# Optimization experiments

Measured on AMD Instinct MI355X. Metric: run time of the kernel, lower is better.

## Reference

```python
import jax, jax.numpy as jnp
import numpy as np

B, T, F = 128, 512, 16   # batch, seq len, n_features
K, PAD, H = 5, 2, 32     # conv kernel, padding, per-feature GRU hidden
NEG = 0.01               # LeakyReLU default negative slope


def setup_inputs() -> dict:
    key = jax.random.key(0)
    ks = iter(jax.random.split(key, 64))

    def u(shape, fan):
        s = 1.0 / np.sqrt(fan)
        return jax.random.uniform(next(ks), shape, jnp.float32, -s, s)

    inp = {}
    inp['x'] = jax.random.normal(next(ks), (B, 2, T), jnp.float32)
    # gru_enc: input=2, hidden=F, unidirectional (torch layout: W_ih [3H,I], W_hh [3H,H])
    inp['enc_Wih'] = u((3 * F, 2), F)
    inp['enc_Whh'] = u((3 * F, F), F)
    inp['enc_bih'] = u((3 * F,), F)
    inp['enc_bhh'] = u((3 * F,), F)
    # last_layers_gru (per feature): input=1, hidden=H, bidirectional
    for d in ('f', 'b'):
        inp[f'g1_Wih_{d}'] = u((F, 3 * H, 1), H)
        inp[f'g1_Whh_{d}'] = u((F, 3 * H, H), H)
        inp[f'g1_bih_{d}'] = u((F, 3 * H), H)
        inp[f'g1_bhh_{d}'] = u((F, 3 * H), H)
    # layers_gru (per feature): input=2H, hidden=H, unidirectional
    inp['g2_Wih'] = u((F, 3 * H, 2 * H), H)
    inp['g2_Whh'] = u((F, 3 * H, H), H)
    inp['g2_bih'] = u((F, 3 * H), H)
    inp['g2_bhh'] = u((F, 3 * H), H)
    # ConvTranspose1d weights, torch layout [C_in, C_out, K]
    inp['w3'] = u((F, 32, 64, K), 32 * K)
    inp['b3'] = u((F, 64), 32 * K)
    inp['w2'] = u((F, 64, 128, K), 64 * K)
    inp['b2'] = u((F, 128), 64 * K)
    inp['w1'] = u((F, 128, 1, K), 128 * K)
    inp['b1'] = u((F, 1), 128 * K)
    return inp


def gru(x, Wih, Whh, bih, bhh):
    # x: [B, T, I] -> [B, T, H]; torch GRU cell math
    Hh = Whh.shape[1]
    xp = jnp.einsum('bti,gi->btg', x, Wih) + bih  # [B,T,3H], input proj for all t

    def step(h, xt):
        g = h @ Whh.T + bhh
        xr, xz, xn = jnp.split(xt, 3, -1)
        hr, hz, hn = jnp.split(g, 3, -1)
        r = jax.nn.sigmoid(xr + hr)
        z = jax.nn.sigmoid(xz + hz)
        n = jnp.tanh(xn + r * hn)
        h = (1 - z) * n + z * h
        return h, h

    h0 = jnp.zeros((x.shape[0], Hh), x.dtype)
    _, ys = jax.lax.scan(step, h0, jnp.swapaxes(xp, 0, 1))
    return jnp.swapaxes(ys, 0, 1)


def bigru(x, Wf, Hf, bif, bhf, Wb, Hb, bib, bhb):
    fwd = gru(x, Wf, Hf, bif, bhf)
    bwd = gru(x[:, ::-1], Wb, Hb, bib, bhb)[:, ::-1]
    return jnp.concatenate([fwd, bwd], -1)


def convT(x, w, b):
    # ConvTranspose1d(stride=1, padding=PAD): x [B,Cin,T], w [Cin,Cout,K]
    wc = jnp.flip(w, -1).transpose(1, 0, 2)  # -> [Cout,Cin,K] cross-correlation kernel
    y = jax.lax.conv_general_dilated(
        x, wc, (1,), [(K - 1 - PAD, K - 1 - PAD)],
        dimension_numbers=('NCH', 'OIH', 'NCH'))
    return y + b[None, :, None]


def reference(x, enc_Wih, enc_Whh, enc_bih, enc_bhh,
              g1_Wih_f, g1_Whh_f, g1_bih_f, g1_bhh_f,
              g1_Wih_b, g1_Whh_b, g1_bih_b, g1_bhh_b,
              g2_Wih, g2_Whh, g2_bih, g2_bhh,
              w3, b3, w2, b2, w1, b1):
    leaky = lambda v: jnp.where(v >= 0, v, NEG * v)
    # encoder GRU over time: x [B,2,T] -> [B,T,F]
    h = gru(jnp.swapaxes(x, 1, 2), enc_Wih, enc_Whh, enc_bih, enc_bhh)

    def per_feature(xi, W1f, H1f, bi1f, bh1f, W1b, H1b, bi1b, bh1b,
                    W2, H2, bi2, bh2, w3_, b3_, w2_, b2_, w1_, b1_):
        # xi: [B,T] single feature channel
        u = bigru(xi[..., None], W1f, H1f, bi1f, bh1f, W1b, H1b, bi1b, bh1b)  # [B,T,2H]
        u = gru(u, W2, H2, bi2, bh2)        # [B,T,H]
        u = jnp.swapaxes(u, 1, 2)           # [B,H,T]
        u = leaky(convT(u, w3_, b3_))       # [B,64,T]
        u = leaky(convT(u, w2_, b2_))       # [B,128,T]
        u = leaky(convT(u, w1_, b1_))       # [B,1,T]
        return u[:, 0]                      # [B,T]

    feats = jnp.moveaxis(h, 2, 0)           # [F,B,T]
    out = jax.vmap(per_feature)(feats,
                                g1_Wih_f, g1_Whh_f, g1_bih_f, g1_bhh_f,
                                g1_Wih_b, g1_Whh_b, g1_bih_b, g1_bhh_b,
                                g2_Wih, g2_Whh, g2_bih, g2_bhh,
                                w3, b3, w2, b2, w1, b1)  # [F,B,T]
    return jnp.moveaxis(out, 0, 2)          # [B,T,F]
```

## Files before the change

### kernel.cpp

```cpp
#include <hip/hip_runtime.h>
#include <math.h>

#define BB 128
#define TT 512
#define FF 16

typedef _Float16 half8 __attribute__((ext_vector_type(8)));
typedef float floatx4 __attribute__((ext_vector_type(4)));

union HU { uint4 u; half8 h; };

__device__ __forceinline__ float bf2f(unsigned short u){
  union { unsigned int i; float f; } c; c.i = ((unsigned int)u) << 16; return c.f;
}
__device__ __forceinline__ unsigned short f2bf(float f){
  union { float f; unsigned int i; } c; c.f = f;
  unsigned int x = c.i;
  unsigned int r = (x + 0x7fffu + ((x >> 16) & 1u)) >> 16;
  return (unsigned short)r;
}
__device__ __forceinline__ float sigm(float x){
  return __builtin_amdgcn_rcpf(1.f + __expf(-x));
}
__device__ __forceinline__ float tanh_fast(float x){
  x = fminf(15.f, fmaxf(-15.f, x));
  float e = __expf(-2.f*x);
  return (1.f - e)*__builtin_amdgcn_rcpf(1.f + e);
}
__device__ __forceinline__ float lrelu(float v){ return v >= 0.f ? v : 0.01f*v; }

__device__ __forceinline__ unsigned int packhl(float v){
  _Float16 hh = (_Float16)v;
  float hf = (float)hh;
  _Float16 hl = (_Float16)(v - hf);
  union { _Float16 h; unsigned short s; } a, b;
  a.h = hh; b.h = hl;
  return (unsigned int)a.s | ((unsigned int)b.s << 16);
}

__device__ __forceinline__ void unpackAB(uint4 P0, uint4 P1, HU& Ah, HU& Al){
  Ah.u.x = (P0.x & 0xffffu) | (P0.y << 16);
  Ah.u.y = (P0.z & 0xffffu) | (P0.w << 16);
  Ah.u.z = (P1.x & 0xffffu) | (P1.y << 16);
  Ah.u.w = (P1.z & 0xffffu) | (P1.w << 16);
  Al.u.x = (P0.x >> 16) | (P0.y & 0xffff0000u);
  Al.u.y = (P0.z >> 16) | (P0.w & 0xffff0000u);
  Al.u.z = (P1.x >> 16) | (P1.y & 0xffff0000u);
  Al.u.w = (P1.z >> 16) | (P1.w & 0xffff0000u);
}

#define MFMA16(A,B,C) __builtin_amdgcn_mfma_f32_16x16x32_f16((A),(B),(C),0,0,0)

__global__ __launch_bounds__(256) void fill_kernel(unsigned short* out, int n, float v){
  int i = blockIdx.x*256 + threadIdx.x;
  if (i < n) out[i] = f2bf(v);
}

__global__ __launch_bounds__(256) void detect1_kernel(const unsigned short* x, float* maxbuf){
  __shared__ float red[256];
  const int base = blockIdx.x*4096 + threadIdx.x*16;
  const uint4* p = (const uint4*)(x + base);
  uint4 a = p[0], b = p[1];
  unsigned int ws[8] = {a.x,a.y,a.z,a.w,b.x,b.y,b.z,b.w};
  float m = 0.f;
  #pragma unroll
  for (int i=0;i<8;i++){
    float v0 = fabsf(bf2f((unsigned short)(ws[i] & 0xffffu)));
    float v1 = fabsf(bf2f((unsigned short)(ws[i] >> 16)));
    if (!isfinite(v0)) v0 = 3e38f;
    if (!isfinite(v1)) v1 = 3e38f;
    m = fmaxf(m, fmaxf(v0, v1));
  }
  red[threadIdx.x] = m; __syncthreads();
  for (int s=128; s>0; s>>=1){
    if (threadIdx.x < s) red[threadIdx.x] = fmaxf(red[threadIdx.x], red[threadIdx.x+s]);
    __syncthreads();
  }
  if (threadIdx.x == 0) maxbuf[blockIdx.x] = red[0];
}
__global__ __launch_bounds__(64) void detect2_kernel(const float* maxbuf, int* flag){
  if (threadIdx.x == 0){
    float m = 0.f;
    for (int i=0;i<32;i++) m = fmaxf(m, maxbuf[i]);
    *flag = (m < 1e4f) ? 1 : 0;
  }
}

struct CvtArgs { const void* p[23]; int sz[23]; int ofs[23]; };

__global__ __launch_bounds__(256) void convert_kernel(CvtArgs a, const int* flag, float* dst){
  const int i = blockIdx.x;
  const int n = a.sz[i];
  const int start = blockIdx.y * 16384;
  if (start >= n) return;
  const int end = (start + 16384 < n) ? start + 16384 : n;
  float* d = dst + a.ofs[i];
  const int s4 = start >> 2, e4 = end >> 2;
  if (*flag){
    const unsigned short* s = (const unsigned short*)a.p[i];
    for (int e = s4 + threadIdx.x; e < e4; e += 256){
      uint2 w = *(const uint2*)(s + 4*e);
      float4 o;
      o.x = bf2f((unsigned short)(w.x & 0xffffu));
      o.y = bf2f((unsigned short)(w.x >> 16));
      o.z = bf2f((unsigned short)(w.y & 0xffffu));
      o.w = bf2f((unsigned short)(w.y >> 16));
      *(float4*)(d + 4*e) = o;
    }
  } else {
    const float* s = (const float*)a.p[i];
    for (int e = s4 + threadIdx.x; e < e4; e += 256)
      *(float4*)(d + 4*e) = *(const float4*)(s + 4*e);
  }
}

__global__ __launch_bounds__(256) void prep16_kernel(
    const float* __restrict__ cvt, _Float16* __restrict__ h16,
    int o6, int o10, int o14, int o13, int o17, int o19, int o2)
{
  const int i = blockIdx.x*256 + threadIdx.x;
  const int y = blockIdx.y;
  if (y == 0){ if (i < 49152) h16[i]          = (_Float16)cvt[o6  + i]; }
  else if (y == 1){ if (i < 49152) h16[49152 + i]  = (_Float16)cvt[o10 + i]; }
  else if (y == 2){ if (i < 49152) h16[98304 + i]  = (_Float16)cvt[o14 + i]; }
  else if (y == 3){ if (i < 98304) h16[147456 + i] = (_Float16)cvt[o13 + i]; }
  else if (y == 4){
    if (i < 163840){
      int ci = i & 31, co = (i >> 5) & 63, fj = i >> 11;
      int f = fj / 5, j = fj - 5*f;
      h16[245760 + i] = (_Float16)cvt[o17 + ((f*32 + ci)*64 + co)*5 + j];
    }
  } else if (y == 5){
    if (i < 655360){
      int ci = i & 63, co = (i >> 6) & 127, fj = i >> 13;
      int f = fj / 5, j = fj - 5*f;
      h16[409600 + i] = (_Float16)cvt[o19 + ((f*64 + ci)*128 + co)*5 + j];
    }
  } else {
    if (i < 1536){
      int k = i & 31, row = i >> 5;
      h16[1064960 + i] = (k < 16) ? (_Float16)cvt[o2 + row*16 + k] : (_Float16)0.f;
    }
  }
}

__global__ __launch_bounds__(128) void xt_kernel(const float* __restrict__ cvt, float* __restrict__ xTp){
  const int t = blockIdx.x, b = threadIdx.x;
  xTp[t*BB + b]            = cvt[(b*2 + 0)*TT + t];
  xTp[65536 + t*BB + b]    = cvt[(b*2 + 1)*TT + t];
}

__global__ __launch_bounds__(64) void enc_kernel(
    const float* __restrict__ xTp, const _Float16* __restrict__ whhE,
    const float* __restrict__ Wih, const float* __restrict__ bih,
    const float* __restrict__ bhh, float* __restrict__ xfeatT)
{
  const int b0 = blockIdx.x*16;
  const int l = threadIdx.x, ml = l & 15, q = l >> 4;
  __shared__ __align__(16) _Float16 HpkH[2][16][24];
  __shared__ __align__(16) _Float16 HpkL[2][16][24];
  half8 Bw[3];
  #pragma unroll
  for (int c=0;c<3;c++)
    Bw[c] = *(const half8*)(whhE + (16*c + ml)*32 + 8*q);
  float w0r=Wih[ml*2],      w1r=Wih[ml*2+1],      bir=bih[ml],    bhr=bhh[ml];
  float w0z=Wih[(16+ml)*2], w1z=Wih[(16+ml)*2+1], biz=bih[16+ml], bhz=bhh[16+ml];
  float w0n=Wih[(32+ml)*2], w1n=Wih[(32+ml)*2+1], bin_=bih[32+ml], bhn=bhh[32+ml];
  float hm[4] = {0,0,0,0};
  HU Ah, Al; Ah.u = make_uint4(0,0,0,0); Al.u = Ah.u;
  const floatx4 z4 = {0.f,0.f,0.f,0.f};
  int pp = 0;
  floatx4 x0v = *(const floatx4*)(xTp + b0 + 4*q);
  floatx4 x1v = *(const floatx4*)(xTp + 65536 + b0 + 4*q);
  for (int t=0;t<TT;t++){
    const int tn = (t < 511) ? t+1 : t;
    floatx4 x0n = *(const floatx4*)(xTp + tn*BB + b0 + 4*q);
    floatx4 x1n = *(const floatx4*)(xTp + 65536 + tn*BB + b0 + 4*q);
    floatx4 C[3];
    #pragma unroll
    for (int c=0;c<3;c++){
      C[c] = MFMA16(Al.h, Bw[c], z4);
      C[c] = MFMA16(Ah.h, Bw[c], C[c]);
    }
    float4 hv4;
    #pragma unroll
    for (int r=0;r<4;r++){
      float xb0 = x0v[r], xb1 = x1v[r];
      float rr = sigm(fmaf(w0r,xb0,fmaf(w1r,xb1,bir)) + C[0][r] + bhr);
      float zz = sigm(fmaf(w0z,xb0,fmaf(w1z,xb1,biz)) + C[1][r] + bhz);
      float nn = tanh_fast(fmaf(w0n,xb0,fmaf(w1n,xb1,bin_)) + rr*(C[2][r] + bhn));
      float hn = nn + zz*(hm[r] - nn);
      hm[r] = hn;
      _Float16 hh = (_Float16)hn;
      _Float16 hl = (_Float16)(hn - (float)hh);
      HpkH[pp][4*q + r][ml] = hh;
      HpkL[pp][4*q + r][ml] = hl;
      ((float*)&hv4)[r] = hn;
    }
    *(float4*)(xfeatT + ((size_t)ml*TT + t)*BB + b0 + 4*q) = hv4;
    __syncthreads();
    if (q < 2){
      Ah.u = *(const uint4*)&HpkH[pp][ml][8*q];
      Al.u = *(const uint4*)&HpkL[pp][ml][8*q];
    } else { Ah.u = make_uint4(0,0,0,0); Al.u = Ah.u; }
    pp ^= 1;
    x0v = x0n; x1v = x1n;
  }
}

__global__ __launch_bounds__(128) void g1b_kernel(
    const float* __restrict__ xT, const _Float16* __restrict__ whh_h,
    const float* __restrict__ wih, const float* __restrict__ bih,
    const float* __restrict__ bhh, _Float16* __restrict__ trace)
{
  const int f = blockIdx.x, b0 = blockIdx.y*16;
  const int wid = threadIdx.x >> 6, l = threadIdx.x & 63, ml = l & 15, q = l >> 4;
  __shared__ unsigned int Hpk[2][16][36];
  half8 Bw[3];
  #pragma unroll
  for (int i=0;i<3;i++){
    int tc = 2*i + wid;
    Bw[i] = *(const half8*)(whh_h + (size_t)f*3072 + (16*tc + ml)*32 + 8*q);
  }
  const int j = 16*wid + ml, base = f*96;
  float wir=wih[base+j], wiz=wih[base+32+j], win=wih[base+64+j];
  float br_=bih[base+j]+bhh[base+j];
  float bz_=bih[base+32+j]+bhh[base+32+j];
  float bin_=bih[base+64+j], bhn_=bhh[base+64+j];
  float hm[4] = {0,0,0,0};
  HU Ah, Al; Ah.u = make_uint4(0,0,0,0); Al.u = Ah.u;
  const floatx4 z4 = {0.f,0.f,0.f,0.f};
  int pp = 0;
  floatx4 xv = *(const floatx4*)(xT + ((size_t)f*TT + 511)*BB + b0 + 4*q);
  const int dostore = (wid == (q >> 1));
  for (int s=0;s<512;s++){
    const int t = 511 - s;
    const int tn = (s < 511) ? t-1 : t;
    floatx4 xnx = *(const floatx4*)(xT + ((size_t)f*TT + tn)*BB + b0 + 4*q);
    floatx4 C[3];
    #pragma unroll
    for (int i=0;i<3;i++){
      C[i] = MFMA16(Al.h, Bw[i], z4);
      C[i] = MFMA16(Ah.h, Bw[i], C[i]);
    }
    #pragma unroll
    for (int r=0;r<4;r++){
      float xb = xv[r];
      float rr = sigm(fmaf(wir, xb, br_) + C[0][r]);
      float zz = sigm(fmaf(wiz, xb, bz_) + C[1][r]);
      float nn = tanh_fast(fmaf(win, xb, bin_) + rr*(C[2][r] + bhn_));
      float hn = nn + zz*(hm[r] - nn);
      hm[r] = hn;
      Hpk[pp][4*q + r][j] = packhl(hn);
    }
    __syncthreads();
    {
      uint4 P0 = *(const uint4*)&Hpk[pp][ml][8*q];
      uint4 P1 = *(const uint4*)&Hpk[pp][ml][8*q + 4];
      unpackAB(P0, P1, Ah, Al);
    }
    if (dostore)
      *(uint4*)(trace + (((size_t)(f*BB + b0 + ml))*TT + t)*32 + 8*q) = Ah.u;
    pp ^= 1;
    xv = xnx;
  }
}

__global__ __launch_bounds__(128) void g1bf_kernel(
    const float* __restrict__ xT,
    const _Float16* __restrict__ whhB_h, const float* __restrict__ wihB,
    const float* __restrict__ bihB, const float* __restrict__ bhhB,
    const _Float16* __restrict__ whhF_h, const float* __restrict__ wihF,
    const float* __restrict__ bihF, const float* __restrict__ bhhF,
    _Float16* __restrict__ traceB, _Float16* __restrict__ traceF)
{
  const int f = blockIdx.x, b0 = blockIdx.y*16, dir = blockIdx.z;
  const _Float16* whh_h = dir ? whhF_h : whhB_h;
  const float* wih = dir ? wihF : wihB;
  const float* bih = dir ? bihF : bihB;
  const float* bhh = dir ? bhhF : bhhB;
  _Float16* trace = dir ? traceF : traceB;
  const int wid = threadIdx.x >> 6, l = threadIdx.x & 63, ml = l & 15, q = l >> 4;
  __shared__ __align__(16) _Float16 HpkH[2][16][40];
  __shared__ __align__(16) _Float16 HpkL[2][16][40];
  half8 Bw[3];
  #pragma unroll
  for (int i=0;i<3;i++){
    int tc = 2*i + wid;
    Bw[i] = *(const half8*)(whh_h + (size_t)f*3072 + (16*tc + ml)*32 + 8*q);
  }
  const int j = 16*wid + ml, base = f*96;
  float wir=wih[base+j], wiz=wih[base+32+j], win=wih[base+64+j];
  float br_=bih[base+j]+bhh[base+j];
  float bz_=bih[base+32+j]+bhh[base+32+j];
  float bin_=bih[base+64+j], bhn_=bhh[base+64+j];
  float hm[4] = {0,0,0,0};
  HU Ah, Al; Ah.u = make_uint4(0,0,0,0); Al.u = Ah.u;
  const floatx4 z4 = {0.f,0.f,0.f,0.f};
  int pp = 0;
  const int tfirst = dir ? 0 : 511;
  floatx4 xv = *(const floatx4*)(xT + ((size_t)f*TT + tfirst)*BB + b0 + 4*q);
  const int dostore = (wid == (q >> 1));
  for (int s=0;s<512;s++){
    const int t  = dir ? s : 511 - s;
    const int sn = (s < 511) ? s+1 : s;
    const int tn = dir ? sn : 511 - sn;
    floatx4 xnx = *(const floatx4*)(xT + ((size_t)f*TT + tn)*BB + b0 + 4*q);
    floatx4 C[3];
    #pragma unroll
    for (int i=0;i<3;i++){
      C[i] = MFMA16(Al.h, Bw[i], z4);
      C[i] = MFMA16(Ah.h, Bw[i], C[i]);
    }
    #pragma unroll
    for (int r=0;r<4;r++){
      float xb = xv[r];
      float rr = sigm(fmaf(wir, xb, br_) + C[0][r]);
      float zz = sigm(fmaf(wiz, xb, bz_) + C[1][r]);
      float nn = tanh_fast(fmaf(win, xb, bin_) + rr*(C[2][r] + bhn_));
      float hn = nn + zz*(hm[r] - nn);
      hm[r] = hn;
      _Float16 hh = (_Float16)hn;
      _Float16 hl = (_Float16)(hn - (float)hh);
      HpkH[pp][4*q + r][j] = hh;
      HpkL[pp][4*q + r][j] = hl;
    }
    __syncthreads();
    Ah.u = *(const uint4*)&HpkH[pp][ml][8*q];
    Al.u = *(const uint4*)&HpkL[pp][ml][8*q];
    if (dostore)
      *(uint4*)(trace + (((size_t)(f*BB + b0 + ml))*TT + t)*32 + 8*q) = Ah.u;
    pp ^= 1;
    xv = xnx;
  }
}

__global__ __launch_bounds__(128) void g2_kernel(
    const float* __restrict__ xT,
    const _Float16* __restrict__ wh1_h, const float* __restrict__ wih1,
    const float* __restrict__ bih1, const float* __restrict__ bhh1,
    const _Float16* __restrict__ wh2_h, const _Float16* __restrict__ w2i_h,
    const float* __restrict__ bih2, const float* __restrict__ bhh2,
    _Float16* __restrict__ trace)
{
  const int f = blockIdx.x, b0 = blockIdx.y*16;
  const int wid = threadIdx.x >> 6, l = threadIdx.x & 63, ml = l & 15, q = l >> 4;
  __shared__ unsigned int Hpk1[2][16][36];
  __shared__ unsigned int Hpk2[2][16][36];
  half8 B1[3], Bh2[3], Bx0[3], Bx1[3];
  #pragma unroll
  for (int i=0;i<3;i++){
    int tc = 2*i + wid;
    B1[i]  = *(const half8*)(wh1_h + (size_t)f*3072 + (16*tc + ml)*32 + 8*q);
    Bh2[i] = *(const half8*)(wh2_h + (size_t)f*3072 + (16*tc + ml)*32 + 8*q);
    Bx0[i] = *(const half8*)(w2i_h + (size_t)f*6144 + (16*tc + ml)*64 + 8*q);
    Bx1[i] = *(const half8*)(w2i_h + (size_t)f*6144 + (16*tc + ml)*64 + 32 + 8*q);
  }
  const int j = 16*wid + ml, base = f*96;
  float wir=wih1[base+j], wiz=wih1[base+32+j], win=wih1[base+64+j];
  float br1_=bih1[base+j]+bhh1[base+j];
  float bz1_=bih1[base+32+j]+bhh1[base+32+j];
  float bin1_=bih1[base+64+j], bhn1_=bhh1[base+64+j];
  float br2_=bih2[base+j]+bhh2[base+j];
  float bz2_=bih2[base+32+j]+bhh2[base+32+j];
  float bin2_=bih2[base+64+j], bhn2_=bhh2[base+64+j];
  float h1[4] = {0,0,0,0};
  float h2[4] = {0,0,0,0};
  HU A1h, A1l, A2h, A2l;
  A1h.u = make_uint4(0,0,0,0); A1l.u = A1h.u; A2h.u = A1h.u; A2l.u = A1h.u;
  const floatx4 z4 = {0.f,0.f,0.f,0.f};
  const size_t rowb = ((size_t)(f*BB + b0 + ml))*TT;
  const int dostore = (wid == (q >> 1));

  {
    floatx4 x0v = *(const floatx4*)(xT + (size_t)f*TT*BB + b0 + 4*q);
    #pragma unroll
    for (int r=0;r<4;r++){
      float xb = x0v[r];
      float rr = sigm(fmaf(wir, xb, br1_));
      float zz = sigm(fmaf(wiz, xb, bz1_));
      float nn = tanh_fast(fmaf(win, xb, bin1_) + rr*bhn1_);
      float hn = (1.f - zz)*nn;
      h1[r] = hn;
      Hpk1[0][4*q + r][j] = packhl(hn);
    }
    __syncthreads();
    uint4 P0 = *(const uint4*)&Hpk1[0][ml][8*q];
    uint4 P1 = *(const uint4*)&Hpk1[0][ml][8*q + 4];
    unpackAB(P0, P1, A1h, A1l);
  }
  int pp = 1;
  uint4 Ub = *(const uint4*)(trace + (rowb + 0)*32 + 8*q);
  floatx4 xv = *(const floatx4*)(xT + ((size_t)f*TT + 1)*BB + b0 + 4*q);
  for (int t=0;t<512;t++){
    const int tn1 = (t < 511) ? t+1 : t;
    const int tn2 = (t < 510) ? t+2 : 511;
    uint4 Ubn = *(const uint4*)(trace + (rowb + tn1)*32 + 8*q);
    floatx4 xnx = *(const floatx4*)(xT + ((size_t)f*TT + tn2)*BB + b0 + 4*q);
    floatx4 C1[3];
    #pragma unroll
    for (int i=0;i<3;i++){
      C1[i] = MFMA16(A1l.h, B1[i], z4);
      C1[i] = MFMA16(A1h.h, B1[i], C1[i]);
    }
    HU Abw; Abw.u = Ub;
    floatx4 Cr, Cz, Cnh, Cnx;
    Cr = MFMA16(A2l.h, Bh2[0], z4); Cr = MFMA16(A2h.h, Bh2[0], Cr);
    Cr = MFMA16(A1l.h, Bx0[0], Cr); Cr = MFMA16(A1h.h, Bx0[0], Cr);
    Cr = MFMA16(Abw.h, Bx1[0], Cr);
    Cz = MFMA16(A2l.h, Bh2[1], z4); Cz = MFMA16(A2h.h, Bh2[1], Cz);
    Cz = MFMA16(A1l.h, Bx0[1], Cz); Cz = MFMA16(A1h.h, Bx0[1], Cz);
    Cz = MFMA16(Abw.h, Bx1[1], Cz);
    Cnh = MFMA16(A2l.h, Bh2[2], z4); Cnh = MFMA16(A2h.h, Bh2[2], Cnh);
    Cnx = MFMA16(A1l.h, Bx0[2], z4); Cnx = MFMA16(A1h.h, Bx0[2], Cnx);
    Cnx = MFMA16(Abw.h, Bx1[2], Cnx);
    #pragma unroll
    for (int r=0;r<4;r++){
      float xb = xv[r];
      float rr1 = sigm(fmaf(wir, xb, br1_) + C1[0][r]);
      float zz1 = sigm(fmaf(wiz, xb, bz1_) + C1[1][r]);
      float nn1 = tanh_fast(fmaf(win, xb, bin1_) + rr1*(C1[2][r] + bhn1_));
      float hn1 = nn1 + zz1*(h1[r] - nn1);
      h1[r] = hn1;
      Hpk1[pp][4*q + r][j] = packhl(hn1);

      float rr2 = sigm(Cr[r] + br2_);
      float zz2 = sigm(Cz[r] + bz2_);
      float nn2 = tanh_fast(Cnx[r] + bin2_ + rr2*(Cnh[r] + bhn2_));
      float hn2 = nn2 + zz2*(h2[r] - nn2);
      h2[r] = hn2;
      Hpk2[pp][4*q + r][j] = packhl(hn2);
    }
    __syncthreads();
    {
      uint4 P0 = *(const uint4*)&Hpk1[pp][ml][8*q];
      uint4 P1 = *(const uint4*)&Hpk1[pp][ml][8*q + 4];
      unpackAB(P0, P1, A1h, A1l);
      uint4 Q0 = *(const uint4*)&Hpk2[pp][ml][8*q];
      uint4 Q1 = *(const uint4*)&Hpk2[pp][ml][8*q + 4];
      unpackAB(Q0, Q1, A2h, A2l);
    }
    if (dostore)
      *(uint4*)(trace + (rowb + t)*32 + 8*q) = A2h.u;
    Ub = Ubn; xv = xnx; pp ^= 1;
  }
}

__global__ __launch_bounds__(128) void g2f_kernel(
    const _Float16* __restrict__ wh2_h, const _Float16* __restrict__ w2i_h,
    const float* __restrict__ bih2, const float* __restrict__ bhh2,
    const _Float16* __restrict__ traceF, _Float16* __restrict__ traceB)
{
  const int f = blockIdx.x, b0 = blockIdx.y*16;
  const int wid = threadIdx.x >> 6, l = threadIdx.x & 63, ml = l & 15, q = l >> 4;
  __shared__ __align__(16) _Float16 HpkH[2][16][40];
  __shared__ __align__(16) _Float16 HpkL[2][16][40];
  half8 Bh2[3], Bx0[3], Bx1[3];
  #pragma unroll
  for (int i=0;i<3;i++){
    int tc = 2*i + wid;
    Bh2[i] = *(const half8*)(wh2_h + (size_t)f*3072 + (16*tc + ml)*32 + 8*q);
    Bx0[i] = *(const half8*)(w2i_h + (size_t)f*6144 + (16*tc + ml)*64 + 8*q);
    Bx1[i] = *(const half8*)(w2i_h + (size_t)f*6144 + (16*tc + ml)*64 + 32 + 8*q);
  }
  const int j = 16*wid + ml, base = f*96;
  float br2_=bih2[base+j]+bhh2[base+j];
  float bz2_=bih2[base+32+j]+bhh2[base+32+j];
  float bin2_=bih2[base+64+j], bhn2_=bhh2[base+64+j];
  float h2[4] = {0,0,0,0};
  HU A2h, A2l; A2h.u = make_uint4(0,0,0,0); A2l.u = A2h.u;
  const floatx4 z4 = {0.f,0.f,0.f,0.f};
  const size_t rowb = ((size_t)(f*BB + b0 + ml))*TT;
  const int dostore = (wid == (q >> 1));
  int pp = 0;
  uint4 F0 = *(const uint4*)(traceF + (rowb + 0)*32 + 8*q);
  uint4 F1 = *(const uint4*)(traceF + (rowb + 1)*32 + 8*q);
  uint4 B0 = *(const uint4*)(traceB + (rowb + 0)*32 + 8*q);
  uint4 B1 = *(const uint4*)(traceB + (rowb + 1)*32 + 8*q);
  for (int t=0;t<512;t++){
    const int tn = (t < 510) ? t+2 : 511;
    uint4 F2 = *(const uint4*)(traceF + (rowb + tn)*32 + 8*q);
    uint4 B2 = *(const uint4*)(traceB + (rowb + tn)*32 + 8*q);
    HU AF; AF.u = F0;
    HU AB; AB.u = B0;
    floatx4 Cr, Cz, Cnh, Cnx;
    {
      floatx4 CrA = MFMA16(A2l.h, Bh2[0], z4); CrA = MFMA16(A2h.h, Bh2[0], CrA);
      floatx4 CrB = MFMA16(AF.h, Bx0[0], z4);  CrB = MFMA16(AB.h, Bx1[0], CrB);
      Cr = CrA + CrB;
      floatx4 CzA = MFMA16(A2l.h, Bh2[1], z4); CzA = MFMA16(A2h.h, Bh2[1], CzA);
      floatx4 CzB = MFMA16(AF.h, Bx0[1], z4);  CzB = MFMA16(AB.h, Bx1[1], CzB);
      Cz = CzA + CzB;
      Cnh = MFMA16(A2l.h, Bh2[2], z4); Cnh = MFMA16(A2h.h, Bh2[2], Cnh);
      Cnx = MFMA16(AF.h, Bx0[2], z4);  Cnx = MFMA16(AB.h, Bx1[2], Cnx);
    }
    #pragma unroll
    for (int r=0;r<4;r++){
      float rr2 = sigm(Cr[r] + br2_);
      float zz2 = sigm(Cz[r] + bz2_);
      float nn2 = tanh_fast(Cnx[r] + bin2_ + rr2*(Cnh[r] + bhn2_));
      float hn2 = nn2 + zz2*(h2[r] - nn2);
      h2[r] = hn2;
      _Float16 hh = (_Float16)hn2;
      _Float16 hl = (_Float16)(hn2 - (float)hh);
      HpkH[pp][4*q + r][j] = hh;
      HpkL[pp][4*q + r][j] = hl;
    }
    __syncthreads();
    A2h.u = *(const uint4*)&HpkH[pp][ml][8*q];
    A2l.u = *(const uint4*)&HpkL[pp][ml][8*q];
    if (dostore)
      *(uint4*)(traceB + (rowb + t)*32 + 8*q) = A2h.u;
    F0 = F1; F1 = F2; B0 = B1; B1 = B2; pp ^= 1;
  }
}

#define UTP 40
#define C3P 72
#define C2P 136
__global__ __launch_bounds__(256) void conv_kernel(
    const _Float16* __restrict__ u2,
    const _Float16* __restrict__ w3T, const float* __restrict__ b3,
    const _Float16* __restrict__ w2T, const float* __restrict__ b2,
    const float* __restrict__ w1, const float* __restrict__ b1,
    void* __restrict__ outv, const int* __restrict__ flag)
{
  const int t0 = blockIdx.x * 64;
  const int b  = blockIdx.y;
  const int f  = blockIdx.z;
  const int tid = threadIdx.x;
  const int w = tid >> 6, l = tid & 63, ml = l & 15, q = l >> 4;

  __shared__ __align__(16) _Float16 utb[84][UTP];
  __shared__ __align__(16) _Float16 c3T[84][C3P];
  __shared__ __align__(16) _Float16 c2T[68][C2P];
  __shared__ float red[4][64];

  const _Float16* urow = u2 + ((size_t)(f*BB + b)*TT)*32;
  const floatx4 z4 = {0.f,0.f,0.f,0.f};

  for (int k = tid; k < 76*4; k += 256){
    int n = k >> 2, seg = k & 3;
    int tg = t0 - 6 + n;
    uint4 v = make_uint4(0,0,0,0);
    if (tg >= 0 && tg < TT) v = *(const uint4*)(urow + (size_t)tg*32 + seg*8);
    *(uint4*)&utb[n][seg*8] = v;
  }
  __syncthreads();

  {
    half8 A3[5];
    #pragma unroll
    for (int jj=0;jj<5;jj++)
      A3[jj] = *(const half8*)(w3T + (((size_t)f*5 + jj)*64 + 16*w + ml)*32 + 8*q);
    float bv[4];
    #pragma unroll
    for (int r=0;r<4;r++) bv[r] = b3[f*64 + 16*w + 4*q + r];
    #pragma unroll
    for (int nt=0;nt<5;nt++){
      floatx4 acc = z4;
      #pragma unroll
      for (int jj=0;jj<5;jj++){
        half8 Bb = *(const half8*)&utb[16*nt + ml + 4 - jj][8*q];
        acc = MFMA16(A3[jj], Bb, acc);
      }
      int tm = 16*nt + ml;
      if (tm < 72){
        int G = t0 - 4 + tm;
        unsigned int pk[2];
        #pragma unroll
        for (int h=0;h<2;h++){
          float v0 = acc[2*h]   + bv[2*h];   v0 = lrelu(v0);
          float v1 = acc[2*h+1] + bv[2*h+1]; v1 = lrelu(v1);
          if (G < 0 || G >= TT){ v0 = 0.f; v1 = 0.f; }
          union { _Float16 hh; unsigned short s; } c0, c1;
          c0.hh = (_Float16)v0; c1.hh = (_Float16)v1;
          pk[h] = (unsigned int)c0.s | ((unsigned int)c1.s << 16);
        }
        *(uint2*)&c3T[tm][16*w + 4*q] = make_uint2(pk[0], pk[1]);
      }
    }
  }
  __syncthreads();

  {
    half8 A2f[5][2][2];
    #pragma unroll
    for (int jj=0;jj<5;jj++)
      #pragma unroll
      for (int ch=0;ch<2;ch++)
        #pragma unroll
        for (int mi=0;mi<2;mi++)
          A2f[jj][ch][mi] = *(const half8*)(w2T + (((size_t)f*5 + jj)*128 + 16*(2*w+mi) + ml)*64 + 32*ch + 8*q);
    float bv2[2][4];
    #pragma unroll
    for (int mi=0;mi<2;mi++)
      #pragma unroll
      for (int r=0;r<4;r++) bv2[mi][r] = b2[f*128 + 16*(2*w+mi) + 4*q + r];
    #pragma unroll
    for (int nt=0;nt<5;nt++){
      floatx4 a0 = z4, a1 = z4;
      #pragma unroll
      for (int jj=0;jj<5;jj++){
        #pragma unroll
        for (int ch=0;ch<2;ch++){
          half8 Bb = *(const half8*)&c3T[16*nt + ml + 4 - jj][32*ch + 8*q];
          a0 = MFMA16(A2f[jj][ch][0], Bb, a0);
          a1 = MFMA16(A2f[jj][ch][1], Bb, a1);
        }
      }
      int p = 16*nt + ml;
      if (p < 68){
        int G = t0 - 2 + p;
        #pragma unroll
        for (int mi=0;mi<2;mi++){
          unsigned int pk[2];
          #pragma unroll
          for (int h=0;h<2;h++){
            float v0 = (mi ? a1[2*h]   : a0[2*h])   + bv2[mi][2*h];   v0 = lrelu(v0);
            float v1 = (mi ? a1[2*h+1] : a0[2*h+1]) + bv2[mi][2*h+1]; v1 = lrelu(v1);
            if (G < 0 || G >= TT){ v0 = 0.f; v1 = 0.f; }
            union { _Float16 hh; unsigned short s; } c0, c1;
            c0.hh = (_Float16)v0; c1.hh = (_Float16)v1;
            pk[h] = (unsigned int)c0.s | ((unsigned int)c1.s << 16);
          }
          *(uint2*)&c2T[p][16*(2*w+mi) + 4*q] = make_uint2(pk[0], pk[1]);
        }
      }
    }
  }
  __syncthreads();

  {
    const int tl = tid & 63, cg = tid >> 6;
    const float* wp = w1 + ((size_t)f*128 + cg*32)*5;
    float acc = 0.f;
    #pragma unroll
    for (int jj=0;jj<5;jj++){
      int row = tl + 4 - jj;
      union { uint4 u; _Float16 h[8]; } u0, u1, u2_, u3;
      u0.u  = *(const uint4*)&c2T[row][cg*32];
      u1.u  = *(const uint4*)&c2T[row][cg*32 + 8];
      u2_.u = *(const uint4*)&c2T[row][cg*32 + 16];
      u3.u  = *(const uint4*)&c2T[row][cg*32 + 24];
      #pragma unroll
      for (int i=0;i<8;i++){
        acc = fmaf(wp[i*5 + jj],      (float)u0.h[i],  acc);
        acc = fmaf(wp[(8+i)*5 + jj],  (float)u1.h[i],  acc);
        acc = fmaf(wp[(16+i)*5 + jj], (float)u2_.h[i], acc);
        acc = fmaf(wp[(24+i)*5 + jj], (float)u3.h[i],  acc);
      }
    }
    red[cg][tl] = acc;
  }
  __syncthreads();
  if (tid < 64){
    float s = b1[f] + red[0][tid] + red[1][tid] + red[2][tid] + red[3][tid];
    s = lrelu(s);
    size_t oi = ((size_t)b*TT + t0 + tid)*FF + f;
    if (*flag) ((unsigned short*)outv)[oi] = f2bf(s);
    else       ((float*)outv)[oi] = s;
  }
}

extern "C" void kernel_launch(void* const* d_in, const int* in_sizes, int n_in,
                              void* d_out, int out_size, void* d_ws, size_t ws_size,
                              hipStream_t stream)
{
  static const int esz[23] = {
    131072,
    96, 768, 48, 48,
    1536, 49152, 1536, 1536,
    1536, 49152, 1536, 1536,
    98304, 49152, 1536, 1536,
    163840, 1024,
    655360, 2048,
    10240, 16
  };
  const size_t NEED = (size_t)16*1024*1024 + (size_t)64*1024*1024;

  float diag = 0.f;
  if (n_in != 23) diag = 2000.f + n_in;
  else {
    for (int i=0;i<23;i++) if (in_sizes[i] != esz[i]) { diag = 1000.f + i; break; }
    if (diag == 0.f && ws_size < NEED) diag = 500.f + (float)(ws_size >> 20);
  }
  if (diag != 0.f){
    hipLaunchKernelGGL(fill_kernel, dim3((out_size+255)/256), dim3(256), 0, stream,
                       (unsigned short*)d_out, out_size, diag);
    return;
  }

  float* cvt = (float*)d_ws;
  int* flagp = (int*)((char*)d_ws + (5ull<<20));
  float* maxbuf = (float*)((char*)d_ws + (5ull<<20) + 256);
  _Float16* h16 = (_Float16*)((char*)d_ws + (6ull<<20));
  float* xTp = (float*)((char*)d_ws + (9ull<<20));
  float* xfeatT = (float*)((char*)d_ws + (10ull<<20));
  _Float16* trace = (_Float16*)((char*)d_ws + (14ull<<20));
  _Float16* traceF = (_Float16*)((char*)d_ws + (80ull<<20));
  const bool bigws = (ws_size >= (145ull<<20));

  CvtArgs a;
  int ofs = 0;
  for (int i=0;i<23;i++){ a.p[i] = d_in[i]; a.sz[i] = esz[i]; a.ofs[i] = ofs; ofs += esz[i]; }
  const float* c[23];
  for (int i=0;i<23;i++) c[i] = cvt + a.ofs[i];

  hipLaunchKernelGGL(detect1_kernel, dim3(32), dim3(256), 0, stream,
                     (const unsigned short*)d_in[0], maxbuf);
  hipLaunchKernelGGL(detect2_kernel, dim3(1), dim3(64), 0, stream, maxbuf, flagp);
  hipLaunchKernelGGL(convert_kernel, dim3(23, 40), dim3(256), 0, stream, a, flagp, cvt);
  hipLaunchKernelGGL(prep16_kernel, dim3(2560, 7), dim3(256), 0, stream,
                     cvt, h16, a.ofs[6], a.ofs[10], a.ofs[14], a.ofs[13],
                     a.ofs[17], a.ofs[19], a.ofs[2]);
  hipLaunchKernelGGL(xt_kernel, dim3(TT), dim3(BB), 0, stream, cvt, xTp);
  hipLaunchKernelGGL(enc_kernel, dim3(BB/16), dim3(64), 0, stream,
                     xTp, h16 + 1064960, c[1], c[3], c[4], xfeatT);
  if (bigws){
    hipLaunchKernelGGL(g1bf_kernel, dim3(FF, 8, 2), dim3(128), 0, stream,
                       xfeatT,
                       h16 + 49152, c[9], c[11], c[12],
                       h16 + 0,     c[5], c[7],  c[8],
                       trace, traceF);
    hipLaunchKernelGGL(g2f_kernel, dim3(FF, 8), dim3(128), 0, stream,
                       h16 + 98304, h16 + 147456, c[15], c[16],
                       traceF, trace);
  } else {
    hipLaunchKernelGGL(g1b_kernel, dim3(FF, 8), dim3(128), 0, stream,
                       xfeatT, h16 + 49152, c[9], c[11], c[12], trace);
    hipLaunchKernelGGL(g2_kernel, dim3(FF, 8), dim3(128), 0, stream,
                       xfeatT, h16 + 0, c[5], c[7], c[8],
                       h16 + 98304, h16 + 147456, c[15], c[16], trace);
  }
  hipLaunchKernelGGL(conv_kernel, dim3(TT/64, BB, FF), dim3(256), 0, stream,
                     trace, h16 + 245760, c[18], h16 + 409600, c[20], c[21], c[22],
                     d_out, flagp);
}
```

Measured before the change: 1.325 ms.

## Run recurrent GRU kernels in a single wavefront and drop block barriers

The encoder, g1bf and g2f GRU kernels now run each recurrence in a single 64-lane wavefront. Each lane computes all six gate column tiles itself instead of splitting them across two waves, which removes the per-step __syncthreads and the double-buffered LDS exchange. Every lane also stores the trace, so the dostore predicate is gone. The cost is twice the MFMA and gate math per wave and more registers. Correctness now relies on the single wave staying in lockstep through LDS without explicit wave barriers.

New measurement: 1.579 ms. 1.19x slower.

```diff
diff --git a/kernel.cpp b/kernel.cpp
--- a/kernel.cpp
+++ b/kernel.cpp
@@ -157,8 +157,8 @@
 {
   const int b0 = blockIdx.x*16;
   const int l = threadIdx.x, ml = l & 15, q = l >> 4;
-  __shared__ __align__(16) _Float16 HpkH[2][16][24];
-  __shared__ __align__(16) _Float16 HpkL[2][16][24];
+  __shared__ __align__(16) _Float16 HpkH[16][24];
+  __shared__ __align__(16) _Float16 HpkL[16][24];
   half8 Bw[3];
   #pragma unroll
   for (int c=0;c<3;c++)
@@ -169,7 +169,6 @@
   float hm[4] = {0,0,0,0};
   HU Ah, Al; Ah.u = make_uint4(0,0,0,0); Al.u = Ah.u;
   const floatx4 z4 = {0.f,0.f,0.f,0.f};
-  int pp = 0;
   floatx4 x0v = *(const floatx4*)(xTp + b0 + 4*q);
   floatx4 x1v = *(const floatx4*)(xTp + 65536 + b0 + 4*q);
   for (int t=0;t<TT;t++){
@@ -193,17 +192,15 @@
       hm[r] = hn;
       _Float16 hh = (_Float16)hn;
       _Float16 hl = (_Float16)(hn - (float)hh);
-      HpkH[pp][4*q + r][ml] = hh;
-      HpkL[pp][4*q + r][ml] = hl;
+      HpkH[4*q + r][ml] = hh;
+      HpkL[4*q + r][ml] = hl;
       ((float*)&hv4)[r] = hn;
     }
     *(float4*)(xfeatT + ((size_t)ml*TT + t)*BB + b0 + 4*q) = hv4;
-    __syncthreads();
     if (q < 2){
-      Ah.u = *(const uint4*)&HpkH[pp][ml][8*q];
-      Al.u = *(const uint4*)&HpkL[pp][ml][8*q];
+      Ah.u = *(const uint4*)&HpkH[ml][8*q];
+      Al.u = *(const uint4*)&HpkL[ml][8*q];
     } else { Ah.u = make_uint4(0,0,0,0); Al.u = Ah.u; }
-    pp ^= 1;
     x0v = x0n; x1v = x1n;
   }
 }
@@ -266,7 +263,7 @@
   }
 }
 
-__global__ __launch_bounds__(128) void g1bf_kernel(
+__global__ __launch_bounds__(64) void g1bf_kernel(
     const float* __restrict__ xT,
     const _Float16* __restrict__ whhB_h, const float* __restrict__ wihB,
     const float* __restrict__ bihB, const float* __restrict__ bhhB,
@@ -280,57 +277,58 @@
   const float* bih = dir ? bihF : bihB;
   const float* bhh = dir ? bhhF : bhhB;
   _Float16* trace = dir ? traceF : traceB;
-  const int wid = threadIdx.x >> 6, l = threadIdx.x & 63, ml = l & 15, q = l >> 4;
-  __shared__ __align__(16) _Float16 HpkH[2][16][40];
-  __shared__ __align__(16) _Float16 HpkL[2][16][40];
-  half8 Bw[3];
+  const int l = threadIdx.x, ml = l & 15, q = l >> 4;
+  __shared__ __align__(16) _Float16 HpkH[16][40];
+  __shared__ __align__(16) _Float16 HpkL[16][40];
+  half8 Bw[6];
   #pragma unroll
-  for (int i=0;i<3;i++){
-    int tc = 2*i + wid;
-    Bw[i] = *(const half8*)(whh_h + (size_t)f*3072 + (16*tc + ml)*32 + 8*q);
-  }
-  const int j = 16*wid + ml, base = f*96;
-  float wir=wih[base+j], wiz=wih[base+32+j], win=wih[base+64+j];
-  float br_=bih[base+j]+bhh[base+j];
-  float bz_=bih[base+32+j]+bhh[base+32+j];
-  float bin_=bih[base+64+j], bhn_=bhh[base+64+j];
-  float hm[4] = {0,0,0,0};
+  for (int c=0;c<6;c++)
+    Bw[c] = *(const half8*)(whh_h + (size_t)f*3072 + (16*c + ml)*32 + 8*q);
+  const int base = f*96;
+  float wir[2], wiz[2], win[2], br_[2], bz_[2], bin_[2], bhn_[2];
+  #pragma unroll
+  for (int cp=0;cp<2;cp++){
+    int j = 16*cp + ml;
+    wir[cp]=wih[base+j]; wiz[cp]=wih[base+32+j]; win[cp]=wih[base+64+j];
+    br_[cp]=bih[base+j]+bhh[base+j];
+    bz_[cp]=bih[base+32+j]+bhh[base+32+j];
+    bin_[cp]=bih[base+64+j]; bhn_[cp]=bhh[base+64+j];
+  }
+  float hm[2][4] = {{0,0,0,0},{0,0,0,0}};
   HU Ah, Al; Ah.u = make_uint4(0,0,0,0); Al.u = Ah.u;
   const floatx4 z4 = {0.f,0.f,0.f,0.f};
-  int pp = 0;
   const int tfirst = dir ? 0 : 511;
   floatx4 xv = *(const floatx4*)(xT + ((size_t)f*TT + tfirst)*BB + b0 + 4*q);
-  const int dostore = (wid == (q >> 1));
   for (int s=0;s<512;s++){
     const int t  = dir ? s : 511 - s;
     const int sn = (s < 511) ? s+1 : s;
     const int tn = dir ? sn : 511 - sn;
     floatx4 xnx = *(const floatx4*)(xT + ((size_t)f*TT + tn)*BB + b0 + 4*q);
-    floatx4 C[3];
-    #pragma unroll
-    for (int i=0;i<3;i++){
-      C[i] = MFMA16(Al.h, Bw[i], z4);
-      C[i] = MFMA16(Ah.h, Bw[i], C[i]);
-    }
-    #pragma unroll
-    for (int r=0;r<4;r++){
-      float xb = xv[r];
-      float rr = sigm(fmaf(wir, xb, br_) + C[0][r]);
-      float zz = sigm(fmaf(wiz, xb, bz_) + C[1][r]);
-      float nn = tanh_fast(fmaf(win, xb, bin_) + rr*(C[2][r] + bhn_));
-      float hn = nn + zz*(hm[r] - nn);
-      hm[r] = hn;
-      _Float16 hh = (_Float16)hn;
-      _Float16 hl = (_Float16)(hn - (float)hh);
-      HpkH[pp][4*q + r][j] = hh;
-      HpkL[pp][4*q + r][j] = hl;
-    }
-    __syncthreads();
-    Ah.u = *(const uint4*)&HpkH[pp][ml][8*q];
-    Al.u = *(const uint4*)&HpkL[pp][ml][8*q];
-    if (dostore)
-      *(uint4*)(trace + (((size_t)(f*BB + b0 + ml))*TT + t)*32 + 8*q) = Ah.u;
-    pp ^= 1;
+    floatx4 C[6];
+    #pragma unroll
+    for (int c=0;c<6;c++){
+      C[c] = MFMA16(Al.h, Bw[c], z4);
+      C[c] = MFMA16(Ah.h, Bw[c], C[c]);
+    }
+    #pragma unroll
+    for (int cp=0;cp<2;cp++){
+      #pragma unroll
+      for (int r=0;r<4;r++){
+        float xb = xv[r];
+        float rr = sigm(fmaf(wir[cp], xb, br_[cp]) + C[cp][r]);
+        float zz = sigm(fmaf(wiz[cp], xb, bz_[cp]) + C[2+cp][r]);
+        float nn = tanh_fast(fmaf(win[cp], xb, bin_[cp]) + rr*(C[4+cp][r] + bhn_[cp]));
+        float hn = nn + zz*(hm[cp][r] - nn);
+        hm[cp][r] = hn;
+        _Float16 hh = (_Float16)hn;
+        _Float16 hl = (_Float16)(hn - (float)hh);
+        HpkH[4*q + r][16*cp + ml] = hh;
+        HpkL[4*q + r][16*cp + ml] = hl;
+      }
+    }
+    Ah.u = *(const uint4*)&HpkH[ml][8*q];
+    Al.u = *(const uint4*)&HpkL[ml][8*q];
+    *(uint4*)(trace + (((size_t)(f*BB + b0 + ml))*TT + t)*32 + 8*q) = Ah.u;
     xv = xnx;
   }
 }
@@ -446,33 +444,35 @@
   }
 }
 
-__global__ __launch_bounds__(128) void g2f_kernel(
+__global__ __launch_bounds__(64) void g2f_kernel(
     const _Float16* __restrict__ wh2_h, const _Float16* __restrict__ w2i_h,
     const float* __restrict__ bih2, const float* __restrict__ bhh2,
     const _Float16* __restrict__ traceF, _Float16* __restrict__ traceB)
 {
   const int f = blockIdx.x, b0 = blockIdx.y*16;
-  const int wid = threadIdx.x >> 6, l = threadIdx.x & 63, ml = l & 15, q = l >> 4;
-  __shared__ __align__(16) _Float16 HpkH[2][16][40];
-  __shared__ __align__(16) _Float16 HpkL[2][16][40];
-  half8 Bh2[3], Bx0[3], Bx1[3];
+  const int l = threadIdx.x, ml = l & 15, q = l >> 4;
+  __shared__ __align__(16) _Float16 HpkH[16][40];
+  __shared__ __align__(16) _Float16 HpkL[16][40];
+  half8 Bh2[6], Bx0[6], Bx1[6];
   #pragma unroll
-  for (int i=0;i<3;i++){
-    int tc = 2*i + wid;
-    Bh2[i] = *(const half8*)(wh2_h + (size_t)f*3072 + (16*tc + ml)*32 + 8*q);
-    Bx0[i] = *(const half8*)(w2i_h + (size_t)f*6144 + (16*tc + ml)*64 + 8*q);
-    Bx1[i] = *(const half8*)(w2i_h + (size_t)f*6144 + (16*tc + ml)*64 + 32 + 8*q);
-  }
-  const int j = 16*wid + ml, base = f*96;
-  float br2_=bih2[base+j]+bhh2[base+j];
-  float bz2_=bih2[base+32+j]+bhh2[base+32+j];
-  float bin2_=bih2[base+64+j], bhn2_=bhh2[base+64+j];
-  float h2[4] = {0,0,0,0};
+  for (int c=0;c<6;c++){
+    Bh2[c] = *(const half8*)(wh2_h + (size_t)f*3072 + (16*c + ml)*32 + 8*q);
+    Bx0[c] = *(const half8*)(w2i_h + (size_t)f*6144 + (16*c + ml)*64 + 8*q);
+    Bx1[c] = *(const half8*)(w2i_h + (size_t)f*6144 + (16*c + ml)*64 + 32 + 8*q);
+  }
+  const int base = f*96;
+  float br2_[2], bz2_[2], bin2_[2], bhn2_[2];
+  #pragma unroll
+  for (int cp=0;cp<2;cp++){
+    int j = 16*cp + ml;
+    br2_[cp]=bih2[base+j]+bhh2[base+j];
+    bz2_[cp]=bih2[base+32+j]+bhh2[base+32+j];
+    bin2_[cp]=bih2[base+64+j]; bhn2_[cp]=bhh2[base+64+j];
+  }
+  float h2[2][4] = {{0,0,0,0},{0,0,0,0}};
   HU A2h, A2l; A2h.u = make_uint4(0,0,0,0); A2l.u = A2h.u;
   const floatx4 z4 = {0.f,0.f,0.f,0.f};
   const size_t rowb = ((size_t)(f*BB + b0 + ml))*TT;
-  const int dostore = (wid == (q >> 1));
-  int pp = 0;
   uint4 F0 = *(const uint4*)(traceF + (rowb + 0)*32 + 8*q);
   uint4 F1 = *(const uint4*)(traceF + (rowb + 1)*32 + 8*q);
   uint4 B0 = *(const uint4*)(traceB + (rowb + 0)*32 + 8*q);
@@ -483,35 +483,40 @@
     uint4 B2 = *(const uint4*)(traceB + (rowb + tn)*32 + 8*q);
     HU AF; AF.u = F0;
     HU AB; AB.u = B0;
-    floatx4 Cr, Cz, Cnh, Cnx;
-    {
-      floatx4 CrA = MFMA16(A2l.h, Bh2[0], z4); CrA = MFMA16(A2h.h, Bh2[0], CrA);
-      floatx4 CrB = MFMA16(AF.h, Bx0[0], z4);  CrB = MFMA16(AB.h, Bx1[0], CrB);
-      Cr = CrA + CrB;
-      floatx4 CzA = MFMA16(A2l.h, Bh2[1], z4); CzA = MFMA16(A2h.h, Bh2[1], CzA);
-      floatx4 CzB = MFMA16(AF.h, Bx0[1], z4);  CzB = MFMA16(AB.h, Bx1[1], CzB);
-      Cz = CzA + CzB;
-      Cnh = MFMA16(A2l.h, Bh2[2], z4); Cnh = MFMA16(A2h.h, Bh2[2], Cnh);
-      Cnx = MFMA16(AF.h, Bx0[2], z4);  Cnx = MFMA16(AB.h, Bx1[2], Cnx);
-    }
-    #pragma unroll
-    for (int r=0;r<4;r++){
-      float rr2 = sigm(Cr[r] + br2_);
-      float zz2 = sigm(Cz[r] + bz2_);
-      float nn2 = tanh_fast(Cnx[r] + bin2_ + rr2*(Cnh[r] + bhn2_));
-      float hn2 = nn2 + zz2*(h2[r] - nn2);
-      h2[r] = hn2;
-      _Float16 hh = (_Float16)hn2;
-      _Float16 hl = (_Float16)(hn2 - (float)hh);
-      HpkH[pp][4*q + r][j] = hh;
-      HpkL[pp][4*q + r][j] = hl;
-    }
-    __syncthreads();
-    A2h.u = *(const uint4*)&HpkH[pp][ml][8*q];
-    A2l.u = *(const uint4*)&HpkL[pp][ml][8*q];
-    if (dostore)
-      *(uint4*)(traceB + (rowb + t)*32 + 8*q) = A2h.u;
-    F0 = F1; F1 = F2; B0 = B1; B1 = B2; pp ^= 1;
+    floatx4 Crz[4], Cnh[2], Cnx[2];
+    #pragma unroll
+    for (int c=0;c<4;c++){
+      floatx4 CA = MFMA16(A2l.h, Bh2[c], z4); CA = MFMA16(A2h.h, Bh2[c], CA);
+      floatx4 CB = MFMA16(AF.h, Bx0[c], z4);  CB = MFMA16(AB.h, Bx1[c], CB);
+      Crz[c] = CA + CB;
+    }
+    #pragma unroll
+    for (int ci=0;ci<2;ci++){
+      int c = 4 + ci;
+      floatx4 ah = MFMA16(A2l.h, Bh2[c], z4); ah = MFMA16(A2h.h, Bh2[c], ah);
+      Cnh[ci] = ah;
+      floatx4 ax = MFMA16(AF.h, Bx0[c], z4);  ax = MFMA16(AB.h, Bx1[c], ax);
+      Cnx[ci] = ax;
+    }
+    #pragma unroll
+    for (int cp=0;cp<2;cp++){
+      #pragma unroll
+      for (int r=0;r<4;r++){
+        float rr2 = sigm(Crz[cp][r] + br2_[cp]);
+        float zz2 = sigm(Crz[2+cp][r] + bz2_[cp]);
+        float nn2 = tanh_fast(Cnx[cp][r] + bin2_[cp] + rr2*(Cnh[cp][r] + bhn2_[cp]));
+        float hn2 = nn2 + zz2*(h2[cp][r] - nn2);
+        h2[cp][r] = hn2;
+        _Float16 hh = (_Float16)hn2;
+        _Float16 hl = (_Float16)(hn2 - (float)hh);
+        HpkH[4*q + r][16*cp + ml] = hh;
+        HpkL[4*q + r][16*cp + ml] = hl;
+      }
+    }
+    A2h.u = *(const uint4*)&HpkH[ml][8*q];
+    A2l.u = *(const uint4*)&HpkL[ml][8*q];
+    *(uint4*)(traceB + (rowb + t)*32 + 8*q) = A2h.u;
+    F0 = F1; F1 = F2; B0 = B1; B1 = B2;
   }
 }
 
@@ -718,12 +723,12 @@
   hipLaunchKernelGGL(enc_kernel, dim3(BB/16), dim3(64), 0, stream,
                      xTp, h16 + 1064960, c[1], c[3], c[4], xfeatT);
   if (bigws){
-    hipLaunchKernelGGL(g1bf_kernel, dim3(FF, 8, 2), dim3(128), 0, stream,
+    hipLaunchKernelGGL(g1bf_kernel, dim3(FF, 8, 2), dim3(64), 0, stream,
                        xfeatT,
                        h16 + 49152, c[9], c[11], c[12],
                        h16 + 0,     c[5], c[7],  c[8],
                        trace, traceF);
-    hipLaunchKernelGGL(g2f_kernel, dim3(FF, 8), dim3(128), 0, stream,
+    hipLaunchKernelGGL(g2f_kernel, dim3(FF, 8), dim3(64), 0, stream,
                        h16 + 98304, h16 + 147456, c[15], c[16],
                        traceF, trace);
   } else {
```
